# Kernel tuning notes

Measured on AMD Instinct MI355X. Metric: run time of the kernel, lower is better.

## Reference

```python
import jax, jax.numpy as jnp
import numpy as np

N, S, H, FA = 16, 64, 256, 256  # batch, sentences, memory_size, fact_attn_hidden


def setup_inputs() -> dict:
    key = jax.random.key(0)
    ks = jax.random.split(key, 12)
    g = lambda k, shp: (jax.random.normal(k, shp, jnp.float32) * 0.05)
    return dict(
        facts=jax.random.normal(ks[0], (N, S, H), jnp.float32),
        prevM=jax.random.normal(ks[1], (N, S, H), jnp.float32),
        questions=jax.random.normal(ks[2], (N, S, H), jnp.float32),
        doc_len=jax.random.randint(ks[3], (N,), S // 2, S + 1),
        z1_w=g(ks[4], (FA, 4 * H)), z1_b=jnp.zeros((FA,), jnp.float32),
        z2_w=g(ks[5], (1, FA)), z2_b=jnp.zeros((1,), jnp.float32),
        Wr_w=g(ks[6], (H, H)), Wr_b=jnp.zeros((H,), jnp.float32),
        Ur_w=g(ks[7], (H, H)), Ur_b=jnp.zeros((H,), jnp.float32),
        W_w=g(ks[8], (H, H)), W_b=jnp.zeros((H,), jnp.float32),
        U_w=g(ks[9], (H, H)), U_b=jnp.zeros((H,), jnp.float32),
        nm_w=g(ks[10], (H, 3 * H)), nm_b=jnp.zeros((H,), jnp.float32),
    )


def reference(facts, prevM, questions, doc_len,
              z1_w, z1_b, z2_w, z2_b,
              Wr_w, Wr_b, Ur_w, Ur_b, W_w, W_b, U_w, U_b,
              nm_w, nm_b):
    n, s, h = facts.shape
    # ---- make_interaction: pairwise features (query axis = dim1, fact/key axis = dim2)
    f = facts[:, None, :, :]       # (N,1,S,H) broadcast over queries
    m = prevM[:, :, None, :]       # (N,S,1,H) broadcast over keys
    q = questions[:, :, None, :]   # (N,S,1,H)
    z = jnp.concatenate([f * q, f * m, jnp.abs(f - q), jnp.abs(f - m)], axis=-1)  # (N,S,S,4H)
    Gh = jnp.tanh(z @ z1_w.T + z1_b)               # (N,S,S,FA)
    G = (Gh @ z2_w.T + z2_b)[..., 0]               # (N,S,S)
    mask = (jnp.arange(s) < doc_len[:, None]).astype(G.dtype)  # (N,S) key mask
    Gm = G * mask[:, None, :]
    Gm = jnp.where(Gm == 0, -jnp.inf, Gm)          # faithful to G[G==0] = -inf
    attn = jax.nn.softmax(Gm, axis=2)              # (N,S,S)

    # ---- AttentionalGRU over the S facts for each of the N*S query rows
    B = n * s
    fb = jnp.broadcast_to(facts[:, None], (n, s, s, h)).reshape(B, s, h)  # (B,S,H)
    gb = attn.reshape(B, s)                                               # (B,S)

    def step(C, xs):
        fact, gt = xs                                   # fact: (B,H), gt: (B,)
        r = jax.nn.sigmoid(fact @ Wr_w.T + Wr_b + C @ Ur_w.T + Ur_b)
        h_t = jnp.tanh(fact @ W_w.T + W_b + r * (C @ U_w.T + U_b))
        gt = gt[:, None]
        return gt * h_t + (1.0 - gt) * C, None

    C0 = jnp.zeros((B, h), facts.dtype)
    C, _ = jax.lax.scan(step, C0, (fb.transpose(1, 0, 2), gb.T))  # scan over S steps
    C = C.reshape(n, s, h)

    # ---- memory update (dropouts are identity in eval mode)
    concat = jnp.concatenate([prevM, C, questions], axis=-1)  # (N,S,3H)
    next_mem = jax.nn.relu(concat @ nm_w.T + nm_b)            # (N,S,H)
    return next_mem, attn
```

## Files before the change

kernel.cpp:

```cpp
#include <hip/hip_runtime.h>
#include <hip/hip_bf16.h>
#include <math.h>

#define NB 16
#define SS 64
#define HH 256
#define FAA 256

using short8 = __attribute__((ext_vector_type(8))) short;
using f32x4  = __attribute__((ext_vector_type(4))) float;

__device__ __forceinline__ float bf2f_u(unsigned int u) {
  union { unsigned int u; float f; } x; x.u = u << 16; return x.f;
}
__device__ __forceinline__ unsigned short f2bf(float f) {
  union { float f; unsigned int u; } x; x.f = f;
  unsigned int u = x.u;
  return (unsigned short)((u + 0x7FFFu + ((u >> 16) & 1u)) >> 16);
}
__device__ __forceinline__ unsigned int cvtpk(float a, float b) {
  unsigned int r;
  asm("v_cvt_pk_bf16_f32 %0, %1, %2" : "=v"(r) : "v"(a), "v"(b));
  return r;
}
__device__ __forceinline__ float sel4(const f32x4 a, int q) {
  const float s01 = (q & 1) ? a[1] : a[0];
  const float s23 = (q & 1) ? a[3] : a[2];
  return (q & 2) ? s23 : s01;
}

__global__ void prolog_cvt(const float* __restrict__ z1w, const float* __restrict__ Ur,
                           const float* __restrict__ U, const float* __restrict__ nmw,
                           const float* __restrict__ pm, const float* __restrict__ qs,
                           unsigned short* __restrict__ z1wbf, unsigned short* __restrict__ wcatbf,
                           unsigned short* __restrict__ nmbf, unsigned short* __restrict__ pmbf,
                           unsigned short* __restrict__ qbf) {
  int idx = blockIdx.x * 256 + threadIdx.x;
  if (idx < 262144) { z1wbf[idx] = f2bf(z1w[idx]); return; }
  idx -= 262144;
  if (idx < 131072) {
    int o = idx >> 8, s = idx & 255;
    int t = s & 31;
    int cc = (s & ~31) + (t >> 1) + ((t & 1) << 4);
    wcatbf[idx] = f2bf(o < 256 ? Ur[o * 256 + cc] : U[(o - 256) * 256 + cc]);
    return;
  }
  idx -= 131072;
  if (idx < 196608) {
    int o = idx / 768, k = idx - o * 768;
    int kk = k;
    if (k >= 256 && k < 512) {
      int s = k - 256, t = s & 31;
      kk = 256 + (s & ~31) + (t >> 1) + ((t & 1) << 4);
    }
    nmbf[idx] = f2bf(nmw[o * 768 + kk]);
    return;
  }
  idx -= 196608;
  if (idx < 262144) { pmbf[idx] = f2bf(pm[idx]); return; }
  idx -= 262144;
  if (idx < 262144) { qbf[idx] = f2bf(qs[idx]); return; }
}

__global__ __launch_bounds__(256) void fact_proj(
    const float* __restrict__ facts, const float* __restrict__ Wr, const float* __restrict__ Wrb,
    const float* __restrict__ Urb, const float* __restrict__ Ww, const float* __restrict__ Wb,
    float* __restrict__ FWr, float* __restrict__ FW) {
  __shared__ float fl[4][HH];
  const int b0 = blockIdx.x * 4;
  const int tid = threadIdx.x;
#pragma unroll
  for (int r = 0; r < 4; ++r) fl[r][tid] = facts[(b0 + r) * HH + tid];
  __syncthreads();
  float ar[4] = {0.f, 0.f, 0.f, 0.f}, aw[4] = {0.f, 0.f, 0.f, 0.f};
  const float4* wr = (const float4*)(Wr + tid * HH);
  const float4* ww = (const float4*)(Ww + tid * HH);
  for (int d4 = 0; d4 < 64; ++d4) {
    float4 a = wr[d4], b = ww[d4];
#pragma unroll
    for (int r = 0; r < 4; ++r) {
      float4 f = *(const float4*)&fl[r][d4 * 4];
      ar[r] += a.x * f.x + a.y * f.y + a.z * f.z + a.w * f.w;
      aw[r] += b.x * f.x + b.y * f.y + b.z * f.z + b.w * f.w;
    }
  }
  const float br = Wrb[tid] + Urb[tid], bw = Wb[tid];
#pragma unroll
  for (int r = 0; r < 4; ++r) {
    FWr[(b0 + r) * HH + tid] = ar[r] + br;
    FW[(b0 + r) * HH + tid] = aw[r] + bw;
  }
}

__global__ __launch_bounds__(512, 2) void gate_gemm(
    const float* __restrict__ facts, const float* __restrict__ prevM,
    const float* __restrict__ questions, const unsigned short* __restrict__ z1wbf,
    const float* __restrict__ z1b, const float* __restrict__ z2w,
    const float* __restrict__ z2b, const int* __restrict__ doc_len,
    float* __restrict__ attn) {
  __shared__ unsigned short A[128][136];
  __shared__ float Gpart[128][4];
  const int bi = blockIdx.x;
  const int n = bi >> 5, i0 = (bi & 31) * 2;
  const int tid = threadIdx.x;
  const int w = tid >> 6, l = tid & 63;
  const int rg = w >> 2, cg = w & 3;
  const int l15 = l & 15, q = l >> 4;
  const int hh2 = (tid & 15) * 2, jb = tid >> 4;

  const float* fn = facts + n * SS * HH;
  const float* qn = questions + (n * SS + i0) * HH;
  const float* mn = prevM + (n * SS + i0) * HH;

  const f32x4 zero4 = {0.f, 0.f, 0.f, 0.f};
  f32x4 acc[4][4];
#pragma unroll
  for (int a = 0; a < 4; ++a)
#pragma unroll
    for (int b = 0; b < 4; ++b) acc[a][b] = zero4;

  float2 fv0, fv1, qv0, qv1, mv0, mv1;
  auto prefetch = [&](int hc) {
    const int h = hc * 32 + hh2;
    fv0 = *(const float2*)(fn + jb * HH + h);
    fv1 = *(const float2*)(fn + (jb + 32) * HH + h);
    qv0 = *(const float2*)(qn + h);
    qv1 = *(const float2*)(qn + HH + h);
    mv0 = *(const float2*)(mn + h);
    mv1 = *(const float2*)(mn + HH + h);
  };
  prefetch(0);

  for (int hc = 0; hc < 8; ++hc) {
    short8 Bf[4][4];
    const unsigned short* bb = z1wbf + (cg * 64 + l15) * 1024 + hc * 32 + q * 8;
#pragma unroll
    for (int s = 0; s < 4; ++s)
#pragma unroll
      for (int nf = 0; nf < 4; ++nf)
        Bf[s][nf] = *(const short8*)(bb + (nf * 16) * 1024 + s * 256);

    {
      float2 fl2[2] = {fv0, fv1}, ql2[2] = {qv0, qv1}, ml2[2] = {mv0, mv1};
#pragma unroll
      for (int pl = 0; pl < 2; ++pl) {
        const int j = jb + pl * 32;
#pragma unroll
        for (int il = 0; il < 2; ++il) {
          const int row = il * 64 + j;
          const float fx = fl2[pl].x, fy = fl2[pl].y;
          const float qx = ql2[il].x, qy = ql2[il].y;
          const float mx = ml2[il].x, my = ml2[il].y;
          *(unsigned int*)&A[row][0 * 32 + hh2] = cvtpk(fx * qx, fy * qy);
          *(unsigned int*)&A[row][1 * 32 + hh2] = cvtpk(fx * mx, fy * my);
          *(unsigned int*)&A[row][2 * 32 + hh2] = cvtpk(fabsf(fx - qx), fabsf(fy - qy));
          *(unsigned int*)&A[row][3 * 32 + hh2] = cvtpk(fabsf(fx - mx), fabsf(fy - my));
        }
      }
    }
    if (hc < 7) prefetch(hc + 1);
    __syncthreads();

#pragma unroll
    for (int s = 0; s < 4; ++s) {
      short8 Af[4];
#pragma unroll
      for (int mf = 0; mf < 4; ++mf)
        Af[mf] = *(const short8*)&A[rg * 64 + mf * 16 + l15][s * 32 + q * 8];
#pragma unroll
      for (int mf = 0; mf < 4; ++mf)
#pragma unroll
        for (int nf = 0; nf < 4; ++nf)
          acc[mf][nf] = __builtin_amdgcn_mfma_f32_16x16x32_bf16(Af[mf], Bf[s][nf], acc[mf][nf], 0, 0, 0);
    }
    __syncthreads();
  }

  float psum[4][4];
#pragma unroll
  for (int mf = 0; mf < 4; ++mf)
#pragma unroll
    for (int v = 0; v < 4; ++v) psum[mf][v] = 0.f;

#pragma unroll
  for (int nf = 0; nf < 4; ++nf) {
    const int k = cg * 64 + nf * 16 + l15;
    const float zb = z1b[k], zw = z2w[k];
#pragma unroll
    for (int mf = 0; mf < 4; ++mf)
#pragma unroll
      for (int v = 0; v < 4; ++v) {
        const float x = acc[mf][nf][v] + zb;
        const float e = __expf(2.f * x);
        const float t = 1.f - 2.f / (e + 1.f);
        psum[mf][v] += zw * t;
      }
  }
#pragma unroll
  for (int d = 1; d < 16; d <<= 1)
#pragma unroll
    for (int mf = 0; mf < 4; ++mf)
#pragma unroll
      for (int v = 0; v < 4; ++v) psum[mf][v] += __shfl_xor(psum[mf][v], d, 64);
  if (l15 == 0) {
#pragma unroll
    for (int mf = 0; mf < 4; ++mf)
#pragma unroll
      for (int v = 0; v < 4; ++v)
        Gpart[rg * 64 + mf * 16 + q * 4 + v][cg] = psum[mf][v];
  }
  __syncthreads();
  if (tid < 128) {
    const float gg = Gpart[tid][0] + Gpart[tid][1] + Gpart[tid][2] + Gpart[tid][3] + z2b[0];
    const int i = i0 + (tid >> 6), j = tid & 63;
    const int dl = doc_len[n];
    const float x = (j < dl && gg != 0.0f) ? gg : -INFINITY;
    float mx = x;
#pragma unroll
    for (int d = 1; d < 64; d <<= 1) mx = fmaxf(mx, __shfl_xor(mx, d, 64));
    const float e = (x == -INFINITY) ? 0.f : __expf(x - mx);
    float s = e;
#pragma unroll
    for (int d = 1; d < 64; d <<= 1) s += __shfl_xor(s, d, 64);
    attn[(n * SS + i) * SS + j] = e / s;
  }
}

__global__ __launch_bounds__(512, 2) void gru_scan(
    const unsigned short* __restrict__ wcat, const float* __restrict__ FWr,
    const float* __restrict__ FW, const float* __restrict__ Ub,
    const float* __restrict__ attn, unsigned short* __restrict__ Cout) {
  __shared__ unsigned short Cbf[2][4 * 272];
  __shared__ float attn_sT[64 * 4];

  const int bi = blockIdx.x, n = bi >> 4, i0 = (bi & 15) * 4;
  const int tid = threadIdx.x, w = tid >> 6, l = tid & 63;
  const int l15 = l & 15, q = l >> 4;
  const int h0 = w * 32 + l15;

  short8 Bf[8][4];
#pragma unroll
  for (int f = 0; f < 4; ++f) {
    const int wrow = ((f >> 1) ? 256 : 0) + w * 32 + (f & 1) * 16 + l15;
    const unsigned short* bb = wcat + wrow * 256 + q * 8;
#pragma unroll
    for (int kt = 0; kt < 8; ++kt)
      Bf[kt][f] = *(const short8*)(bb + kt * 32);
  }

  const float ub0 = Ub[h0], ub1 = Ub[h0 + 16];

  for (int e = tid; e < 64 * 4; e += 512)
    attn_sT[e] = attn[(n * SS + i0 + (e & 3)) * SS + (e >> 2)];
  for (int e = tid; e < 544; e += 512)
    ((unsigned int*)Cbf[0])[e] = 0u;
  __syncthreads();

  const float* fwr_g = FWr + n * SS * HH;
  const float* fw_g  = FW + n * SS * HH;

  float cm0 = 0.f, cm1 = 0.f;
  float fr0 = fwr_g[h0], fr1 = fwr_g[h0 + 16];
  float fc0 = fw_g[h0],  fc1 = fw_g[h0 + 16];

  for (int t = 0; t < 64; ++t) {
    const int cur = t & 1;
    const unsigned short* Cr = Cbf[cur];
    unsigned int* Cw = (unsigned int*)Cbf[cur ^ 1];

    short8 Af[8];
    const int arow = (l15 & 3) * 272;
#pragma unroll
    for (int kt = 0; kt < 8; ++kt)
      Af[kt] = *(const short8*)&Cr[arow + kt * 32 + q * 8];

    float nr0 = 0.f, nr1 = 0.f, nc0 = 0.f, nc1 = 0.f;
    if (t < 63) {
      nr0 = fwr_g[(t + 1) * HH + h0];
      nr1 = fwr_g[(t + 1) * HH + h0 + 16];
      nc0 = fw_g[(t + 1) * HH + h0];
      nc1 = fw_g[(t + 1) * HH + h0 + 16];
    }

    const f32x4 z4 = {0.f, 0.f, 0.f, 0.f};
    f32x4 acc[4];
#pragma unroll
    for (int f = 0; f < 4; ++f) acc[f] = z4;
    __builtin_amdgcn_s_setprio(1);
#pragma unroll
    for (int kt = 0; kt < 8; ++kt)
#pragma unroll
      for (int f = 0; f < 4; ++f)
        acc[f] = __builtin_amdgcn_mfma_f32_16x16x32_bf16(Af[kt], Bf[kt][f], acc[f], 0, 0, 0);
    __builtin_amdgcn_s_setprio(0);

    const float yr0 = sel4(acc[0], q), yr1 = sel4(acc[1], q);
    const float yu0 = sel4(acc[2], q), yu1 = sel4(acc[3], q);
    const float g = attn_sT[t * 4 + q];

    const float r0 = 1.f / (1.f + __expf(-(fr0 + yr0)));
    const float x0 = fc0 + r0 * (yu0 + ub0);
    const float e0 = __expf(2.f * x0);
    const float h0t = 1.f - 2.f / (e0 + 1.f);
    cm0 += g * (h0t - cm0);

    const float r1 = 1.f / (1.f + __expf(-(fr1 + yr1)));
    const float x1 = fc1 + r1 * (yu1 + ub1);
    const float e1 = __expf(2.f * x1);
    const float h1t = 1.f - 2.f / (e1 + 1.f);
    cm1 += g * (h1t - cm1);

    Cw[q * 136 + w * 16 + l15] = cvtpk(cm0, cm1);

    fr0 = nr0; fr1 = nr1; fc0 = nc0; fc1 = nc1;
    __syncthreads();
  }

  {
    const int row = tid >> 7, wo = tid & 127;
    ((unsigned int*)Cout)[(n * SS + i0 + row) * 128 + wo] =
        *(const unsigned int*)&Cbf[0][row * 272 + wo * 2];
  }
}

__global__ __launch_bounds__(256) void next_mem_gemm(
    const unsigned short* __restrict__ pmbf, const unsigned short* __restrict__ cbf,
    const unsigned short* __restrict__ qbf, const unsigned short* __restrict__ nmbf,
    const float* __restrict__ nmb, float* __restrict__ out) {
  __shared__ unsigned short A[64][40];
  const int bi = blockIdx.x;
  const int rb = bi >> 2, cb = bi & 3;
  const int r0 = rb * 64, c0 = cb * 64;
  const int tid = threadIdx.x, w = tid >> 6, l = tid & 63;
  const int l15 = l & 15, q = l >> 4;

  f32x4 acc[4];
  const f32x4 z4 = {0.f, 0.f, 0.f, 0.f};
#pragma unroll
  for (int nf = 0; nf < 4; ++nf) acc[nf] = z4;

  for (int kt = 0; kt < 24; ++kt) {
    const int kg = kt * 32;
    const unsigned short* src =
        kg < 256 ? (pmbf + kg) : (kg < 512 ? (cbf + kg - 256) : (qbf + kg - 512));
    const int kk = (tid & 15) * 2;
#pragma unroll
    for (int ps = 0; ps < 4; ++ps) {
      const int row = ps * 16 + (tid >> 4);
      *(unsigned int*)&A[row][kk] = *(const unsigned int*)(src + (r0 + row) * HH + kk);
    }
    __syncthreads();
    short8 Bfr[4];
#pragma unroll
    for (int nf = 0; nf < 4; ++nf)
      Bfr[nf] = *(const short8*)(nmbf + (c0 + nf * 16 + l15) * 768 + kg + q * 8);
    const short8 Af = *(const short8*)&A[w * 16 + l15][q * 8];
#pragma unroll
    for (int nf = 0; nf < 4; ++nf)
      acc[nf] = __builtin_amdgcn_mfma_f32_16x16x32_bf16(Af, Bfr[nf], acc[nf], 0, 0, 0);
    __syncthreads();
  }
#pragma unroll
  for (int nf = 0; nf < 4; ++nf) {
    const int col = c0 + nf * 16 + l15;
    const float bv = nmb[col];
#pragma unroll
    for (int v = 0; v < 4; ++v) {
      const int grow = r0 + w * 16 + q * 4 + v;
      out[grow * HH + col] = fmaxf(acc[nf][v] + bv, 0.f);
    }
  }
}

extern "C" void kernel_launch(void* const* d_in, const int* in_sizes, int n_in,
                              void* d_out, int out_size, void* d_ws, size_t ws_size,
                              hipStream_t stream) {
  const float* facts     = (const float*)d_in[0];
  const float* prevM     = (const float*)d_in[1];
  const float* questions = (const float*)d_in[2];
  const int*   doc_len   = (const int*)d_in[3];
  const float* z1w = (const float*)d_in[4];
  const float* z1b = (const float*)d_in[5];
  const float* z2w = (const float*)d_in[6];
  const float* z2b = (const float*)d_in[7];
  const float* Wrw = (const float*)d_in[8];
  const float* Wrb = (const float*)d_in[9];
  const float* Urw = (const float*)d_in[10];
  const float* Urb = (const float*)d_in[11];
  const float* Ww  = (const float*)d_in[12];
  const float* Wb  = (const float*)d_in[13];
  const float* Uw  = (const float*)d_in[14];
  const float* Ub  = (const float*)d_in[15];
  const float* nmw = (const float*)d_in[16];
  const float* nmb = (const float*)d_in[17];

  char* ws = (char*)d_ws;
  unsigned short* z1wbf  = (unsigned short*)(ws + 0);
  unsigned short* wcatbf = (unsigned short*)(ws + 524288);
  unsigned short* nmbf   = (unsigned short*)(ws + 786432);
  unsigned short* pmbf   = (unsigned short*)(ws + 1179648);
  unsigned short* qbf    = (unsigned short*)(ws + 1703936);
  float* FWr = (float*)(ws + 2490368);
  float* FW  = (float*)(ws + 3538944);
  unsigned short* cbf = (unsigned short*)(ws + 4587520);

  float* out  = (float*)d_out;
  float* attn = out + NB * SS * HH;

  prolog_cvt<<<4352, 256, 0, stream>>>(z1w, Urw, Uw, nmw, prevM, questions,
                                       z1wbf, wcatbf, nmbf, pmbf, qbf);
  fact_proj<<<256, 256, 0, stream>>>(facts, Wrw, Wrb, Urb, Ww, Wb, FWr, FW);
  gate_gemm<<<512, 512, 0, stream>>>(facts, prevM, questions, z1wbf, z1b, z2w, z2b,
                                     doc_len, attn);
  gru_scan<<<256, 512, 0, stream>>>(wcatbf, FWr, FW, Ub, attn, cbf);
  next_mem_gemm<<<64, 256, 0, stream>>>(pmbf, cbf, qbf, nmbf, nmb, out);
}
```

Baseline: 273.4 us.

## Double-buffer gate GEMM with async LDS weight staging and swizzled tiles

Restructures gate_gemm into a per-K-slice double-buffered pipeline. The z1 weight tile is staged into LDS via global_load_lds with an XOR swizzle, and the next A tile is built while MFMAs run on the current buffer. It also raises launch_bounds occupancy to 4 and adds setprio around the MFMA bursts. The aim is to drop the large per-iteration register B-fragment loads and overlap global/LDS traffic with compute, at the cost of more barriers per iteration. Separately, next_mem_gemm is split into narrower 32-column tiles to double the block count.

Result: faster. 244.8 us (-10.5%).

```diff
diff --git a/kernel.cpp b/kernel.cpp
--- a/kernel.cpp
+++ b/kernel.cpp
@@ -10,9 +10,6 @@
 using short8 = __attribute__((ext_vector_type(8))) short;
 using f32x4  = __attribute__((ext_vector_type(4))) float;
 
-__device__ __forceinline__ float bf2f_u(unsigned int u) {
-  union { unsigned int u; float f; } x; x.u = u << 16; return x.f;
-}
 __device__ __forceinline__ unsigned short f2bf(float f) {
   union { float f; unsigned int u; } x; x.f = f;
   unsigned int u = x.u;
@@ -92,26 +89,62 @@
   }
 }
 
-__global__ __launch_bounds__(512, 2) void gate_gemm(
+__global__ __launch_bounds__(512, 4) void gate_gemm(
     const float* __restrict__ facts, const float* __restrict__ prevM,
     const float* __restrict__ questions, const unsigned short* __restrict__ z1wbf,
     const float* __restrict__ z1b, const float* __restrict__ z2w,
     const float* __restrict__ z2b, const int* __restrict__ doc_len,
     float* __restrict__ attn) {
-  __shared__ unsigned short A[128][136];
+  __shared__ unsigned short Ab[2][128 * 32];
+  __shared__ unsigned short Bb[2][256 * 32];
   __shared__ float Gpart[128][4];
+
   const int bi = blockIdx.x;
   const int n = bi >> 5, i0 = (bi & 31) * 2;
   const int tid = threadIdx.x;
   const int w = tid >> 6, l = tid & 63;
   const int rg = w >> 2, cg = w & 3;
   const int l15 = l & 15, q = l >> 4;
-  const int hh2 = (tid & 15) * 2, jb = tid >> 4;
+  const int t15 = tid & 15, jb = tid >> 4;
 
   const float* fn = facts + n * SS * HH;
   const float* qn = questions + (n * SS + i0) * HH;
   const float* mn = prevM + (n * SS + i0) * HH;
 
+  auto stageB = [&](int buf, int hc, int s) {
+    const int kb = s * 256 + hc * 32;
+    const int swz = ((l & 3) ^ ((l >> 2) & 3)) * 8;
+#pragma unroll
+    for (int j = 0; j < 2; ++j) {
+      const int colg = w * 32 + j * 16 + (l >> 2);
+      const unsigned short* src = z1wbf + colg * 1024 + kb + swz;
+      __builtin_amdgcn_global_load_lds(src, Bb[buf] + (w * 32 + j * 16) * 32, 16, 0, 0);
+    }
+  };
+
+  auto buildA = [&](int buf, int s, float2 f0, float2 f1, float2 q0, float2 q1,
+                    float2 m0, float2 m1) {
+    unsigned int* dst = (unsigned int*)Ab[buf];
+    const int dsw = t15 ^ ((jb & 3) << 2);
+    const float2 o0 = (s & 1) ? m0 : q0;
+    const float2 o1 = (s & 1) ? m1 : q1;
+#pragma unroll
+    for (int pl = 0; pl < 2; ++pl) {
+      const float fx = pl ? f1.x : f0.x;
+      const float fy = pl ? f1.y : f0.y;
+#pragma unroll
+      for (int il = 0; il < 2; ++il) {
+        const int row = il * 64 + pl * 32 + jb;
+        const float ox = il ? o1.x : o0.x;
+        const float oy = il ? o1.y : o0.y;
+        float a, b;
+        if (s < 2) { a = fx * ox;         b = fy * oy; }
+        else       { a = fabsf(fx - ox);  b = fabsf(fy - oy); }
+        dst[row * 16 + dsw] = cvtpk(a, b);
+      }
+    }
+  };
+
   const f32x4 zero4 = {0.f, 0.f, 0.f, 0.f};
   f32x4 acc[4][4];
 #pragma unroll
@@ -119,61 +152,70 @@
 #pragma unroll
     for (int b = 0; b < 4; ++b) acc[a][b] = zero4;
 
-  float2 fv0, fv1, qv0, qv1, mv0, mv1;
-  auto prefetch = [&](int hc) {
+  auto mfmaStep = [&](int buf) {
+    short8 Bfr[4];
+#pragma unroll
+    for (int nf = 0; nf < 4; ++nf) {
+      const int col = cg * 64 + nf * 16 + l15;
+      Bfr[nf] = *(const short8*)&Bb[buf][col * 32 + (q ^ (l15 & 3)) * 8];
+    }
+    __builtin_amdgcn_s_setprio(1);
+#pragma unroll
+    for (int mf = 0; mf < 4; ++mf) {
+      const int row = rg * 64 + mf * 16 + l15;
+      const short8 Afm = *(const short8*)&Ab[buf][row * 32 + (q ^ (l15 & 3)) * 8];
+#pragma unroll
+      for (int nf = 0; nf < 4; ++nf)
+        acc[mf][nf] = __builtin_amdgcn_mfma_f32_16x16x32_bf16(Afm, Bfr[nf], acc[mf][nf], 0, 0, 0);
+    }
+    __builtin_amdgcn_s_setprio(0);
+  };
+
+  const int hh2 = t15 * 2;
+  auto pf = [&](int hc, float2& f0, float2& f1, float2& q0, float2& q1,
+                float2& m0, float2& m1) {
     const int h = hc * 32 + hh2;
-    fv0 = *(const float2*)(fn + jb * HH + h);
-    fv1 = *(const float2*)(fn + (jb + 32) * HH + h);
-    qv0 = *(const float2*)(qn + h);
-    qv1 = *(const float2*)(qn + HH + h);
-    mv0 = *(const float2*)(mn + h);
-    mv1 = *(const float2*)(mn + HH + h);
+    f0 = *(const float2*)(fn + jb * HH + h);
+    f1 = *(const float2*)(fn + (jb + 32) * HH + h);
+    q0 = *(const float2*)(qn + h);
+    q1 = *(const float2*)(qn + HH + h);
+    m0 = *(const float2*)(mn + h);
+    m1 = *(const float2*)(mn + HH + h);
   };
-  prefetch(0);
-
+
+  float2 Rf0, Rf1, Rq0, Rq1, Rm0, Rm1;
+  float2 Sf0, Sf1, Sq0, Sq1, Sm0, Sm1;
+  pf(0, Rf0, Rf1, Rq0, Rq1, Rm0, Rm1);
+  stageB(0, 0, 0);
+  buildA(0, 0, Rf0, Rf1, Rq0, Rq1, Rm0, Rm1);
+  __syncthreads();
+
+  int buf = 0;
   for (int hc = 0; hc < 8; ++hc) {
-    short8 Bf[4][4];
-    const unsigned short* bb = z1wbf + (cg * 64 + l15) * 1024 + hc * 32 + q * 8;
-#pragma unroll
-    for (int s = 0; s < 4; ++s)
-#pragma unroll
-      for (int nf = 0; nf < 4; ++nf)
-        Bf[s][nf] = *(const short8*)(bb + (nf * 16) * 1024 + s * 256);
-
-    {
-      float2 fl2[2] = {fv0, fv1}, ql2[2] = {qv0, qv1}, ml2[2] = {mv0, mv1};
-#pragma unroll
-      for (int pl = 0; pl < 2; ++pl) {
-        const int j = jb + pl * 32;
-#pragma unroll
-        for (int il = 0; il < 2; ++il) {
-          const int row = il * 64 + j;
-          const float fx = fl2[pl].x, fy = fl2[pl].y;
-          const float qx = ql2[il].x, qy = ql2[il].y;
-          const float mx = ml2[il].x, my = ml2[il].y;
-          *(unsigned int*)&A[row][0 * 32 + hh2] = cvtpk(fx * qx, fy * qy);
-          *(unsigned int*)&A[row][1 * 32 + hh2] = cvtpk(fx * mx, fy * my);
-          *(unsigned int*)&A[row][2 * 32 + hh2] = cvtpk(fabsf(fx - qx), fabsf(fy - qy));
-          *(unsigned int*)&A[row][3 * 32 + hh2] = cvtpk(fabsf(fx - mx), fabsf(fy - my));
-        }
-      }
-    }
-    if (hc < 7) prefetch(hc + 1);
-    __syncthreads();
-
-#pragma unroll
-    for (int s = 0; s < 4; ++s) {
-      short8 Af[4];
-#pragma unroll
-      for (int mf = 0; mf < 4; ++mf)
-        Af[mf] = *(const short8*)&A[rg * 64 + mf * 16 + l15][s * 32 + q * 8];
-#pragma unroll
-      for (int mf = 0; mf < 4; ++mf)
-#pragma unroll
-        for (int nf = 0; nf < 4; ++nf)
-          acc[mf][nf] = __builtin_amdgcn_mfma_f32_16x16x32_bf16(Af[mf], Bf[s][nf], acc[mf][nf], 0, 0, 0);
-    }
-    __syncthreads();
+    stageB(buf ^ 1, hc, 1);
+    buildA(buf ^ 1, 1, Rf0, Rf1, Rq0, Rq1, Rm0, Rm1);
+    mfmaStep(buf);
+    __syncthreads();
+    buf ^= 1;
+    stageB(buf ^ 1, hc, 2);
+    buildA(buf ^ 1, 2, Rf0, Rf1, Rq0, Rq1, Rm0, Rm1);
+    mfmaStep(buf);
+    __syncthreads();
+    buf ^= 1;
+    stageB(buf ^ 1, hc, 3);
+    buildA(buf ^ 1, 3, Rf0, Rf1, Rq0, Rq1, Rm0, Rm1);
+    if (hc < 7) pf(hc + 1, Sf0, Sf1, Sq0, Sq1, Sm0, Sm1);
+    mfmaStep(buf);
+    __syncthreads();
+    buf ^= 1;
+    if (hc < 7) {
+      stageB(buf ^ 1, hc + 1, 0);
+      buildA(buf ^ 1, 0, Sf0, Sf1, Sq0, Sq1, Sm0, Sm1);
+    }
+    mfmaStep(buf);
+    __syncthreads();
+    buf ^= 1;
+    Rf0 = Sf0; Rf1 = Sf1; Rq0 = Sq0; Rq1 = Sq1; Rm0 = Sm0; Rm1 = Sm1;
   }
 
   float psum[4][4];
@@ -329,15 +371,15 @@
     const float* __restrict__ nmb, float* __restrict__ out) {
   __shared__ unsigned short A[64][40];
   const int bi = blockIdx.x;
-  const int rb = bi >> 2, cb = bi & 3;
-  const int r0 = rb * 64, c0 = cb * 64;
+  const int rb = bi >> 3, cb = bi & 7;
+  const int r0 = rb * 64, c0 = cb * 32;
   const int tid = threadIdx.x, w = tid >> 6, l = tid & 63;
   const int l15 = l & 15, q = l >> 4;
 
-  f32x4 acc[4];
+  f32x4 acc[2];
   const f32x4 z4 = {0.f, 0.f, 0.f, 0.f};
 #pragma unroll
-  for (int nf = 0; nf < 4; ++nf) acc[nf] = z4;
+  for (int nf = 0; nf < 2; ++nf) acc[nf] = z4;
 
   for (int kt = 0; kt < 24; ++kt) {
     const int kg = kt * 32;
@@ -350,18 +392,18 @@
       *(unsigned int*)&A[row][kk] = *(const unsigned int*)(src + (r0 + row) * HH + kk);
     }
     __syncthreads();
-    short8 Bfr[4];
-#pragma unroll
-    for (int nf = 0; nf < 4; ++nf)
+    short8 Bfr[2];
+#pragma unroll
+    for (int nf = 0; nf < 2; ++nf)
       Bfr[nf] = *(const short8*)(nmbf + (c0 + nf * 16 + l15) * 768 + kg + q * 8);
     const short8 Af = *(const short8*)&A[w * 16 + l15][q * 8];
 #pragma unroll
-    for (int nf = 0; nf < 4; ++nf)
+    for (int nf = 0; nf < 2; ++nf)
       acc[nf] = __builtin_amdgcn_mfma_f32_16x16x32_bf16(Af, Bfr[nf], acc[nf], 0, 0, 0);
     __syncthreads();
   }
 #pragma unroll
-  for (int nf = 0; nf < 4; ++nf) {
+  for (int nf = 0; nf < 2; ++nf) {
     const int col = c0 + nf * 16 + l15;
     const float bv = nmb[col];
 #pragma unroll
@@ -413,5 +455,5 @@
   gate_gemm<<<512, 512, 0, stream>>>(facts, prevM, questions, z1wbf, z1b, z2w, z2b,
                                      doc_len, attn);
   gru_scan<<<256, 512, 0, stream>>>(wcatbf, FWr, FW, Ub, attn, cbf);
-  next_mem_gemm<<<64, 256, 0, stream>>>(pmbf, cbf, qbf, nmbf, nmb, out);
-}
+  next_mem_gemm<<<128, 256, 0, stream>>>(pmbf, cbf, qbf, nmbf, nmb, out);
+}
```
